# Performance work log

Measured on AMD Instinct MI355X. Metric: run time of the kernel, lower is better.

## Reference

```python
import jax, jax.numpy as jnp
import numpy as np

ALPHA = 1.0          # temperature of the Bayesian DP (init kwarg alpha)
NEG = -1e9           # -inf surrogate, safe in fp32/bf16


def conv1d_same(x, w, b):
    # x: [B, T, Cin], w: [K, Cin, Cout], 'SAME' padding, stride 1
    y = jax.lax.conv_general_dilated(x, w, window_strides=(1,), padding='SAME',
                                     dimension_numbers=('NWC', 'WIO', 'NWC'))
    return y + b


def postnet(x, ws, bs):
    # Tacotron-style conv PostNet: n_conv conv1d layers with tanh (dropout=0, eval mode)
    for w, b in zip(ws, bs):
        x = jnp.tanh(conv1d_same(x, w, b))
    return x


def bayesian_dp(W, alpha):
    """Monotonic-alignment Bayesian DP (Gumbel propagation).

    W: [B, T, S] node weights on the alignment grid (T = mel time, S = text).
    Each node (t, s) has two parents: (t-1, s) [stay] and (t-1, s-1) [advance].
      mu[t,s] = W[t,s] + (1/alpha) * logsumexp(alpha*mu[t-1,s], alpha*mu[t-1,s-1])
      pi[t,s] = softmax over the two parents -> [B, T, S, 2]
    """
    B, T, S = W.shape
    m0 = W[:, 0] + jnp.where(jnp.arange(S) == 0, 0.0, NEG)   # path must start at (0,0)
    pi0 = jnp.broadcast_to(jnp.array([1.0, 0.0], W.dtype), (B, S, 2))

    def step(prev, w_t):
        # prev: [B, S] = mu[t-1]; shifted: mu[t-1, s-1]
        shifted = jnp.concatenate([jnp.full((B, 1), NEG, prev.dtype), prev[:, :-1]], axis=1)
        stacked = jnp.stack([prev, shifted], axis=-1)         # [B, S, 2]
        m = w_t + jax.nn.logsumexp(alpha * stacked, axis=-1) / alpha
        pi_t = jax.nn.softmax(alpha * stacked, axis=-1)
        return m, (m, pi_t)

    _, (ms, pis) = jax.lax.scan(step, m0, jnp.swapaxes(W, 0, 1)[1:])  # scan over T-1
    mu = jnp.concatenate([m0[:, None], jnp.swapaxes(ms, 0, 1)], axis=1)    # [B, T, S]
    pi = jnp.concatenate([pi0[:, None], jnp.swapaxes(pis, 0, 1)], axis=1)  # [B, T, S, 2]
    return mu, pi


def setup_inputs() -> dict:
    key = jax.random.key(0)
    ks = jax.random.split(key, 6)
    B, T, S = 32, 2000, 400
    NMELS, H, K = 80, 256, 5
    inputs = jax.random.normal(ks[0], (B, T, NMELS), dtype=jnp.float32)
    src_enc = jax.random.normal(ks[1], (B, S, H), dtype=jnp.float32)
    mask = jnp.ones((B, T, S), dtype=jnp.float32)
    w1 = jax.random.normal(ks[2], (K, NMELS, H), dtype=jnp.float32) * 0.05
    w2 = jax.random.normal(ks[3], (K, H, H), dtype=jnp.float32) * 0.05
    w3 = jax.random.normal(ks[4], (K, H, H), dtype=jnp.float32) * 0.05
    b1 = jnp.zeros((H,), jnp.float32)
    b2 = jnp.zeros((H,), jnp.float32)
    b3 = jnp.zeros((H,), jnp.float32)
    return {"inputs": inputs, "src_enc": src_enc, "mask": mask,
            "w1": w1, "b1": b1, "w2": w2, "b2": b2, "w3": w3, "b3": b3}


def reference(inputs, src_enc, mask, w1, b1, w2, b2, w3, b3):
    # PostNet over mel frames -> spec embeddings matching src_enc dim
    Wspec = postnet(inputs, [w1, w2, w3], [b1, b2, b3])       # [B, T, H]
    # attention score grid
    W = jnp.einsum('bth,bsh->bts', Wspec, src_enc)            # [B, T, S]
    alignments = jax.nn.softmax(W, axis=1)                    # softmax over mel-time (dim 1)
    mu, pi = bayesian_dp(alignments * mask, ALPHA)
    return mu, pi, alignments, Wspec
```

## Files before the change

kernel.cpp:

```cpp
#include <hip/hip_runtime.h>
#include <hip/hip_bf16.h>

#define B_ 32
#define T_ 2000
#define S_ 400
#define C0_ 80
#define H_ 256

static constexpr float NEGV = -1e9f;
static constexpr int NMU  = B_ * T_ * S_;
static constexpr int NPI  = 2 * NMU;

typedef _Float16 f16x8 __attribute__((ext_vector_type(8)));
typedef float    f32x4 __attribute__((ext_vector_type(4)));

__global__ __launch_bounds__(256)
void wprep(const float* __restrict__ w, _Float16* __restrict__ wcat,
           int CIN, int CPAD)
{
  const int tot = 256 * 5 * CPAD;
  int idx = blockIdx.x * 256 + threadIdx.x;
  if (idx >= tot) return;
  int co  = idx / (5 * CPAD);
  int rem = idx - co * (5 * CPAD);
  int k   = rem / CPAD;
  int ci  = rem - k * CPAD;
  float v = (ci < CIN) ? w[((size_t)k * CIN + ci) * H_ + co] : 0.f;
  wcat[idx] = (_Float16)v;
}

__global__ __launch_bounds__(256)
void ecast(const float* __restrict__ e, _Float16* __restrict__ ef)
{
  const int n4 = B_ * S_ * H_ / 4;
  int idx = blockIdx.x * 256 + threadIdx.x;
  if (idx >= n4) return;
  float4 v = ((const float4*)e)[idx];
  _Float16* d = ef + (size_t)idx * 4;
  d[0] = (_Float16)v.x; d[1] = (_Float16)v.y;
  d[2] = (_Float16)v.z; d[3] = (_Float16)v.w;
}

template<int CIN, int CPAD, bool INF32, bool OUTF32>
__global__ __launch_bounds__(256)
void conv_mfma(const void* __restrict__ xin, const _Float16* __restrict__ wcat,
               const float* __restrict__ bias, void* __restrict__ yout)
{
  constexpr int KK  = 5 * CPAD;
  constexpr int NS  = KK / 32;
  constexpr int STR = CPAD + 8;
  __shared__ _Float16 xs[68 * STR];
  const int b   = blockIdx.y;
  const int t0  = blockIdx.x * 64;
  const int tid = threadIdx.x;
  const int w   = tid >> 6;
  const int l   = tid & 63;

  if constexpr (INF32) {
    const float* xb = (const float*)xin + (size_t)b * T_ * CIN;
    constexpr int NG = CPAD / 4;
    for (int idx = tid; idx < 68 * NG; idx += 256) {
      int j = idx / NG, g = idx - j * NG;
      int t = t0 - 2 + j;
      int c = g * 4;
      float4 v = make_float4(0.f, 0.f, 0.f, 0.f);
      if (t >= 0 && t < T_ && c < CIN) v = *(const float4*)&xb[(size_t)t * CIN + c];
      _Float16* d = &xs[j * STR + c];
      d[0] = (_Float16)v.x; d[1] = (_Float16)v.y;
      d[2] = (_Float16)v.z; d[3] = (_Float16)v.w;
    }
  } else {
    const _Float16* xb = (const _Float16*)xin + (size_t)b * T_ * CIN;
    constexpr int NG = CPAD / 8;
    for (int idx = tid; idx < 68 * NG; idx += 256) {
      int j = idx / NG, g = idx - j * NG;
      int t = t0 - 2 + j;
      f16x8 v = {(_Float16)0,(_Float16)0,(_Float16)0,(_Float16)0,
                 (_Float16)0,(_Float16)0,(_Float16)0,(_Float16)0};
      if (t >= 0 && t < T_) v = *(const f16x8*)&xb[(size_t)t * CIN + g * 8];
      *(f16x8*)&xs[j * STR + g * 8] = v;
    }
  }
  __syncthreads();

  const int lr = l & 15;
  const int lk = (l >> 4) * 8;

  f32x4 acc[4][4];
  const f32x4 zz = {0.f, 0.f, 0.f, 0.f};
#pragma unroll
  for (int i = 0; i < 4; i++)
#pragma unroll
    for (int j = 0; j < 4; j++) acc[i][j] = zz;

  const _Float16* wbase = wcat + (size_t)(w * 64 + lr) * KK + lk;

  for (int kk = 0; kk < NS; kk++) {
    const int p  = kk * 32;
    const int k  = p / CPAD;
    const int ci = p - k * CPAD;
    f16x8 a0 = *(const f16x8*)&xs[( 0 + lr + k) * STR + ci + lk];
    f16x8 a1 = *(const f16x8*)&xs[(16 + lr + k) * STR + ci + lk];
    f16x8 a2 = *(const f16x8*)&xs[(32 + lr + k) * STR + ci + lk];
    f16x8 a3 = *(const f16x8*)&xs[(48 + lr + k) * STR + ci + lk];
    f16x8 w0 = *(const f16x8*)&wbase[(size_t)( 0) * KK + p];
    f16x8 w1 = *(const f16x8*)&wbase[(size_t)(16) * KK + p];
    f16x8 w2 = *(const f16x8*)&wbase[(size_t)(32) * KK + p];
    f16x8 w3 = *(const f16x8*)&wbase[(size_t)(48) * KK + p];
    acc[0][0] = __builtin_amdgcn_mfma_f32_16x16x32_f16(a0, w0, acc[0][0], 0, 0, 0);
    acc[0][1] = __builtin_amdgcn_mfma_f32_16x16x32_f16(a0, w1, acc[0][1], 0, 0, 0);
    acc[0][2] = __builtin_amdgcn_mfma_f32_16x16x32_f16(a0, w2, acc[0][2], 0, 0, 0);
    acc[0][3] = __builtin_amdgcn_mfma_f32_16x16x32_f16(a0, w3, acc[0][3], 0, 0, 0);
    acc[1][0] = __builtin_amdgcn_mfma_f32_16x16x32_f16(a1, w0, acc[1][0], 0, 0, 0);
    acc[1][1] = __builtin_amdgcn_mfma_f32_16x16x32_f16(a1, w1, acc[1][1], 0, 0, 0);
    acc[1][2] = __builtin_amdgcn_mfma_f32_16x16x32_f16(a1, w2, acc[1][2], 0, 0, 0);
    acc[1][3] = __builtin_amdgcn_mfma_f32_16x16x32_f16(a1, w3, acc[1][3], 0, 0, 0);
    acc[2][0] = __builtin_amdgcn_mfma_f32_16x16x32_f16(a2, w0, acc[2][0], 0, 0, 0);
    acc[2][1] = __builtin_amdgcn_mfma_f32_16x16x32_f16(a2, w1, acc[2][1], 0, 0, 0);
    acc[2][2] = __builtin_amdgcn_mfma_f32_16x16x32_f16(a2, w2, acc[2][2], 0, 0, 0);
    acc[2][3] = __builtin_amdgcn_mfma_f32_16x16x32_f16(a2, w3, acc[2][3], 0, 0, 0);
    acc[3][0] = __builtin_amdgcn_mfma_f32_16x16x32_f16(a3, w0, acc[3][0], 0, 0, 0);
    acc[3][1] = __builtin_amdgcn_mfma_f32_16x16x32_f16(a3, w1, acc[3][1], 0, 0, 0);
    acc[3][2] = __builtin_amdgcn_mfma_f32_16x16x32_f16(a3, w2, acc[3][2], 0, 0, 0);
    acc[3][3] = __builtin_amdgcn_mfma_f32_16x16x32_f16(a3, w3, acc[3][3], 0, 0, 0);
  }

#pragma unroll
  for (int ct = 0; ct < 4; ct++) {
    const int co = w * 64 + ct * 16 + lr;
    const float bv = bias[co];
#pragma unroll
    for (int tt = 0; tt < 4; tt++) {
#pragma unroll
      for (int r = 0; r < 4; r++) {
        const int t = t0 + tt * 16 + (l >> 4) * 4 + r;
        if (t < T_) {
          float v = tanhf(acc[tt][ct][r] + bv);
          if constexpr (OUTF32)
            ((float*)yout)[((size_t)b * T_ + t) * H_ + co] = v;
          else
            ((_Float16*)yout)[((size_t)b * T_ + t) * H_ + co] = (_Float16)v;
        }
      }
    }
  }
}

__global__ __launch_bounds__(256)
void einsum_mfma(const float* __restrict__ A, const _Float16* __restrict__ E,
                 float* __restrict__ Wg)
{
  constexpr int STR = H_ + 8;
  __shared__ _Float16 xs[64 * STR];
  const int b   = blockIdx.z;
  const int t0  = blockIdx.x * 64;
  const int s0  = blockIdx.y * 256;
  const int tid = threadIdx.x;
  const int w   = tid >> 6;
  const int l   = tid & 63;

  const float* Ab = A + (size_t)b * T_ * H_;
  for (int idx = tid; idx < 64 * 64; idx += 256) {
    int row = idx >> 6, g = idx & 63;
    int t = t0 + row;
    float4 v = make_float4(0.f, 0.f, 0.f, 0.f);
    if (t < T_) v = *(const float4*)&Ab[(size_t)t * H_ + 4 * g];
    _Float16* d = &xs[row * STR + 4 * g];
    d[0] = (_Float16)v.x; d[1] = (_Float16)v.y;
    d[2] = (_Float16)v.z; d[3] = (_Float16)v.w;
  }
  __syncthreads();

  const int lr = l & 15;
  const int lk = (l >> 4) * 8;

  f32x4 acc[4][4];
  const f32x4 zz = {0.f, 0.f, 0.f, 0.f};
#pragma unroll
  for (int i = 0; i < 4; i++)
#pragma unroll
    for (int j = 0; j < 4; j++) acc[i][j] = zz;

  const _Float16* Eb = E + (size_t)b * S_ * H_;
  const int sr = s0 + w * 64 + lr;
  const _Float16* e0 = Eb + (size_t)((sr      < S_) ? sr      : (S_ - 1)) * H_ + lk;
  const _Float16* e1 = Eb + (size_t)((sr + 16 < S_) ? sr + 16 : (S_ - 1)) * H_ + lk;
  const _Float16* e2 = Eb + (size_t)((sr + 32 < S_) ? sr + 32 : (S_ - 1)) * H_ + lk;
  const _Float16* e3 = Eb + (size_t)((sr + 48 < S_) ? sr + 48 : (S_ - 1)) * H_ + lk;

#pragma unroll
  for (int kk = 0; kk < 8; kk++) {
    const int p = kk * 32;
    f16x8 a0 = *(const f16x8*)&xs[( 0 + lr) * STR + p + lk];
    f16x8 a1 = *(const f16x8*)&xs[(16 + lr) * STR + p + lk];
    f16x8 a2 = *(const f16x8*)&xs[(32 + lr) * STR + p + lk];
    f16x8 a3 = *(const f16x8*)&xs[(48 + lr) * STR + p + lk];
    f16x8 w0 = *(const f16x8*)&e0[p];
    f16x8 w1 = *(const f16x8*)&e1[p];
    f16x8 w2 = *(const f16x8*)&e2[p];
    f16x8 w3 = *(const f16x8*)&e3[p];
    acc[0][0] = __builtin_amdgcn_mfma_f32_16x16x32_f16(a0, w0, acc[0][0], 0, 0, 0);
    acc[0][1] = __builtin_amdgcn_mfma_f32_16x16x32_f16(a0, w1, acc[0][1], 0, 0, 0);
    acc[0][2] = __builtin_amdgcn_mfma_f32_16x16x32_f16(a0, w2, acc[0][2], 0, 0, 0);
    acc[0][3] = __builtin_amdgcn_mfma_f32_16x16x32_f16(a0, w3, acc[0][3], 0, 0, 0);
    acc[1][0] = __builtin_amdgcn_mfma_f32_16x16x32_f16(a1, w0, acc[1][0], 0, 0, 0);
    acc[1][1] = __builtin_amdgcn_mfma_f32_16x16x32_f16(a1, w1, acc[1][1], 0, 0, 0);
    acc[1][2] = __builtin_amdgcn_mfma_f32_16x16x32_f16(a1, w2, acc[1][2], 0, 0, 0);
    acc[1][3] = __builtin_amdgcn_mfma_f32_16x16x32_f16(a1, w3, acc[1][3], 0, 0, 0);
    acc[2][0] = __builtin_amdgcn_mfma_f32_16x16x32_f16(a2, w0, acc[2][0], 0, 0, 0);
    acc[2][1] = __builtin_amdgcn_mfma_f32_16x16x32_f16(a2, w1, acc[2][1], 0, 0, 0);
    acc[2][2] = __builtin_amdgcn_mfma_f32_16x16x32_f16(a2, w2, acc[2][2], 0, 0, 0);
    acc[2][3] = __builtin_amdgcn_mfma_f32_16x16x32_f16(a2, w3, acc[2][3], 0, 0, 0);
    acc[3][0] = __builtin_amdgcn_mfma_f32_16x16x32_f16(a3, w0, acc[3][0], 0, 0, 0);
    acc[3][1] = __builtin_amdgcn_mfma_f32_16x16x32_f16(a3, w1, acc[3][1], 0, 0, 0);
    acc[3][2] = __builtin_amdgcn_mfma_f32_16x16x32_f16(a3, w2, acc[3][2], 0, 0, 0);
    acc[3][3] = __builtin_amdgcn_mfma_f32_16x16x32_f16(a3, w3, acc[3][3], 0, 0, 0);
  }

  float* Wb = Wg + (size_t)b * T_ * S_;
#pragma unroll
  for (int ct = 0; ct < 4; ct++) {
    const int s = s0 + w * 64 + ct * 16 + lr;
    if (s < S_) {
#pragma unroll
      for (int tt = 0; tt < 4; tt++) {
#pragma unroll
        for (int r = 0; r < 4; r++) {
          const int t = t0 + tt * 16 + (l >> 4) * 4 + r;
          if (t < T_) Wb[(size_t)t * S_ + s] = acc[tt][ct][r];
        }
      }
    }
  }
}

__global__ __launch_bounds__(256)
void softmax_stats(const float* __restrict__ Wg, float* __restrict__ statsOut)
{
  const int b  = blockIdx.y;
  const int tx = threadIdx.x & 63;
  const int ty = threadIdx.x >> 6;
  const int s  = blockIdx.x * 64 + tx;
  const bool act = (s < S_);
  float m = -1e30f, l = 0.f;
  if (act) {
    const float* col = Wg + (size_t)b * T_ * S_ + s;
#pragma unroll 4
    for (int t = ty; t < T_; t += 4) {
      float v  = col[(size_t)t * S_];
      float nm = fmaxf(m, v);
      l = l * __expf(m - nm) + __expf(v - nm);
      m = nm;
    }
  }
  __shared__ float rm[4][64], rl[4][64];
  rm[ty][tx] = m; rl[ty][tx] = l;
  __syncthreads();
  if (ty == 0 && act) {
    float M = rm[0][tx];
#pragma unroll
    for (int q = 1; q < 4; q++) M = fmaxf(M, rm[q][tx]);
    float L = 0.f;
#pragma unroll
    for (int q = 0; q < 4; q++) L += rl[q][tx] * __expf(rm[q][tx] - M);
    statsOut[(size_t)b * S_ + s] = M + __logf(L);
  }
}

__global__ __launch_bounds__(256)
void norm_kernel(float* __restrict__ al, const float* __restrict__ Mk,
                 const float* __restrict__ stats, float* __restrict__ wdp)
{
  constexpr float C2 = 1.44269504f;
  const int gid = blockIdx.x * 256 + threadIdx.x;
  if (gid >= NMU / 4) return;
  const int b   = gid / (T_ * S_ / 4);
  const int rem = gid - b * (T_ * S_ / 4);
  const int s4  = rem % (S_ / 4);
  const float4 st4 = *(const float4*)&stats[(size_t)b * S_ + 4 * s4];
  float4 r = ((const float4*)al)[gid];
  float4 k = ((const float4*)Mk)[gid];
  float4 a;
  a.x = __expf(r.x - st4.x);
  a.y = __expf(r.y - st4.y);
  a.z = __expf(r.z - st4.z);
  a.w = __expf(r.w - st4.w);
  ((float4*)al)[gid] = a;
  ((float4*)wdp)[gid] = make_float4(a.x * k.x * C2, a.y * k.y * C2,
                                    a.z * k.z * C2, a.w * k.w * C2);
}

__global__ __launch_bounds__(256, 1)
void dp_skew2(const float* Wdp, float* muOut, float* piOut)
{
  __shared__ float ring[64 * S_];
  __shared__ float bnd[32][4];
  const int b = blockIdx.x;
  const int w = threadIdx.x >> 6;
  const int l = threadIdx.x & 63;
  const int lc = (l < 50) ? l : 49;
  const bool act = (l < 50);
  const int sc = 100 * w + 2 * lc;

  const float* wb  = Wdp   + (size_t)b * T_ * S_;
  float*       mub = muOut + (size_t)b * T_ * S_;
  float*       pib = piOut + (size_t)(2 * b) * T_ * S_;

  constexpr float LN2  = 0.693147181f;
  constexpr float NEGN = -1.44269504e9f;

#define DMA(row)                                                            \
  { const char* s_ = (const char*)(wb + (size_t)(row) * S_);                \
    char* d_ = (char*)ring + (((row) & 63) * 1600);                         \
    __builtin_amdgcn_global_load_lds(                                       \
      (const __attribute__((address_space(1))) void*)(s_ + l * 16),         \
      (__attribute__((address_space(3))) void*)(d_ + l * 16), 16, 0, 0);    \
    if (l < 36)                                                             \
      __builtin_amdgcn_global_load_lds(                                     \
        (const __attribute__((address_space(1))) void*)(s_ + 1024 + l*16),  \
        (__attribute__((address_space(3))) void*)(d_ + 1024 + l*16), 16, 0, 0); }

#pragma unroll
  for (int i = 0; i < 6; ++i) { const int r0 = 6 * w + i; DMA(r0) }
  asm volatile("s_waitcnt vmcnt(0)" ::: "memory");
  __syncthreads();

  float n0 = NEGN, n1 = NEGN;

  for (int p = 0; p <= 253; ++p) {
    __builtin_amdgcn_s_barrier();
    const int j = p - w - 1;

    {
      const int dr = 8 * p + 24 + 2 * w;
      if (dr < T_) DMA(dr)
      const int dr1 = dr + 1;
      if (dr1 < T_) DMA(dr1)
    }

    if (p == w) {
      float2 c0v = *(const float2*)&ring[sc];
      n0 = c0v.x + ((sc == 0) ? 0.f : NEGN);
      n1 = c0v.y + NEGN;
      if (act) {
        *(float2*)&mub[sc] = make_float2(n0 * LN2, n1 * LN2);
        *(float4*)&pib[2 * sc] = make_float4(1.f, 0.f, 1.f, 0.f);
      }
      if (l == 49) bnd[0][w] = n1;
    } else if (j >= 0 && j <= 249) {
      const int tb = 8 * j + 1;
      float2 cur[8];
      float  bq[8];
#pragma unroll
      for (int k = 0; k < 8; ++k) {
        const int t = tb + k;
        cur[k] = (t < T_) ? *(const float2*)&ring[(t & 63) * S_ + sc]
                          : make_float2(0.f, 0.f);
        bq[k] = (w > 0) ? bnd[(t - 1) & 31][w - 1] : NEGN;
      }
      float* mrow = mub + (size_t)tb * S_ + sc;
      float* prow = pib + (size_t)tb * (2 * S_) + 2 * sc;
#pragma unroll
      for (int k = 0; k < 8; ++k) {
        const int t = tb + k;
        if (t < T_) {
          float sh = __shfl_up(n1, 1);
          float sft0 = (l == 0) ? bq[k] : sh;
          float d0 = n0 - sft0;
          float e0; asm("v_exp_f32 %0, %1" : "=v"(e0) : "v"(-fabsf(d0)));
          float q0 = 1.f + e0;
          float lg0; asm("v_log_f32 %0, %1" : "=v"(lg0) : "v"(q0));
          float rc0; asm("v_rcp_f32 %0, %1" : "=v"(rc0) : "v"(q0));
          float p00 = (d0 >= 0.f) ? rc0 : 1.f - rc0;
          float nn0 = cur[k].x + fmaxf(n0, sft0) + lg0;
          float d1 = n1 - n0;
          float e1; asm("v_exp_f32 %0, %1" : "=v"(e1) : "v"(-fabsf(d1)));
          float q1 = 1.f + e1;
          float lg1; asm("v_log_f32 %0, %1" : "=v"(lg1) : "v"(q1));
          float rc1; asm("v_rcp_f32 %0, %1" : "=v"(rc1) : "v"(q1));
          float p01 = (d1 >= 0.f) ? rc1 : 1.f - rc1;
          float nn1 = cur[k].y + fmaxf(n1, n0) + lg1;
          if (act) {
            *(float2*)mrow = make_float2(nn0 * LN2, nn1 * LN2);
            *(float4*)prow = make_float4(p00, 1.f - p00, p01, 1.f - p01);
          }
          n0 = nn0; n1 = nn1;
          if (l == 49) bnd[t & 31][w] = n1;
        }
        mrow += S_;
        prow += 2 * S_;
      }
    }
    asm volatile("s_waitcnt lgkmcnt(0)" ::: "memory");
    asm volatile("s_waitcnt vmcnt(56)" ::: "memory");
  }
#undef DMA
}

extern "C" void kernel_launch(void* const* d_in, const int* in_sizes, int n_in,
                              void* d_out, int out_size, void* d_ws, size_t ws_size,
                              hipStream_t stream)
{
  (void)in_sizes; (void)n_in; (void)out_size; (void)d_ws; (void)ws_size;
  const float* x   = (const float*)d_in[0];
  const float* enc = (const float*)d_in[1];
  const float* msk = (const float*)d_in[2];
  const float* w1  = (const float*)d_in[3];
  const float* b1  = (const float*)d_in[4];
  const float* w2  = (const float*)d_in[5];
  const float* b2  = (const float*)d_in[6];
  const float* w3  = (const float*)d_in[7];
  const float* b3  = (const float*)d_in[8];

  float* out = (float*)d_out;
  float* mu  = out;
  float* pi  = out + NMU;
  float* al  = out + NMU + NPI;
  float* wsp = out + NMU + NPI + NMU;

  _Float16*  h1  = (_Float16*)(pi + 26000000);
  _Float16*  h2  = (_Float16*)(pi + 35000000);
  _Float16*  wc1 = (_Float16*)(pi + 44000000);
  _Float16*  wc2 = (_Float16*)(pi + 44100000);
  _Float16*  wc3 = (_Float16*)(pi + 44300000);
  _Float16*  encf = (_Float16*)(pi + 44600000);
  float*     pistats = pi + NPI - 13056;

  hipLaunchKernelGGL(wprep, dim3((256*5*96 +255)/256), dim3(256), 0, stream, w1, wc1, C0_, 96);
  hipLaunchKernelGGL(wprep, dim3((256*5*256+255)/256), dim3(256), 0, stream, w2, wc2, H_, 256);
  hipLaunchKernelGGL(wprep, dim3((256*5*256+255)/256), dim3(256), 0, stream, w3, wc3, H_, 256);
  hipLaunchKernelGGL(ecast, dim3(B_*S_*H_/4/256), dim3(256), 0, stream, enc, encf);

  dim3 cgrid((T_ + 63) / 64, B_);
  hipLaunchKernelGGL((conv_mfma<C0_,  96, true,  false>), cgrid, dim3(256), 0, stream,
                     (const void*)x,  wc1, b1, (void*)h1);
  hipLaunchKernelGGL((conv_mfma<H_,  256, false, false>), cgrid, dim3(256), 0, stream,
                     (const void*)h1, wc2, b2, (void*)h2);
  hipLaunchKernelGGL((conv_mfma<H_,  256, false, true >), cgrid, dim3(256), 0, stream,
                     (const void*)h2, wc3, b3, (void*)wsp);

  hipLaunchKernelGGL(einsum_mfma, dim3((T_ + 63) / 64, (S_ + 255) / 256, B_), dim3(256),
                     0, stream, wsp, encf, al);
  hipLaunchKernelGGL(softmax_stats, dim3((S_ + 63) / 64, B_), dim3(256), 0, stream, al, pistats);
  hipLaunchKernelGGL(norm_kernel, dim3(NMU / 4 / 256), dim3(256), 0, stream, al, msk, pistats, mu);
  hipLaunchKernelGGL(dp_skew2, dim3(B_), dim3(256), 0, stream, mu, mu, pi);
}
```

Measured before the change: 1.073 ms.

## Fuse softmax column statistics into einsum epilogue with partial max/sum reduction

The einsum kernel now computes per-tile column max and sum-of-exp from its accumulator registers. It combines them across lanes with xor shuffles and writes partial stats for each of the 32 time blocks. A small stats_reduce kernel then merges these partials into a log-sum-exp per (b, s). This removes the separate softmax_stats pass, which reread the whole 25.6M-element score grid with strided column access. It adds exp work and two scratch buffers to the einsum epilogue.

```diff
diff --git a/kernel.cpp b/kernel.cpp
--- a/kernel.cpp
+++ b/kernel.cpp
@@ -148,7 +148,8 @@
 
 __global__ __launch_bounds__(256)
 void einsum_mfma(const float* __restrict__ A, const _Float16* __restrict__ E,
-                 float* __restrict__ Wg)
+                 float* __restrict__ Wg,
+                 float* __restrict__ pm, float* __restrict__ pl)
 {
   constexpr int STR = H_ + 8;
   __shared__ _Float16 xs[64 * STR];
@@ -232,39 +233,61 @@
       }
     }
   }
-}
-
-__global__ __launch_bounds__(256)
-void softmax_stats(const float* __restrict__ Wg, float* __restrict__ statsOut)
-{
-  const int b  = blockIdx.y;
-  const int tx = threadIdx.x & 63;
-  const int ty = threadIdx.x >> 6;
-  const int s  = blockIdx.x * 64 + tx;
-  const bool act = (s < S_);
-  float m = -1e30f, l = 0.f;
-  if (act) {
-    const float* col = Wg + (size_t)b * T_ * S_ + s;
+
+  const int tblk = blockIdx.x;
+#pragma unroll
+  for (int ct = 0; ct < 4; ct++) {
+    float M = -3e38f;
+#pragma unroll
+    for (int tt = 0; tt < 4; tt++)
+#pragma unroll
+      for (int r = 0; r < 4; r++) {
+        const int t = t0 + tt * 16 + (l >> 4) * 4 + r;
+        if (t < T_) M = fmaxf(M, acc[tt][ct][r]);
+      }
+    float L = 0.f;
+#pragma unroll
+    for (int tt = 0; tt < 4; tt++)
+#pragma unroll
+      for (int r = 0; r < 4; r++) {
+        const int t = t0 + tt * 16 + (l >> 4) * 4 + r;
+        if (t < T_) L += __expf(acc[tt][ct][r] - M);
+      }
+#pragma unroll
+    for (int mk = 16; mk <= 32; mk <<= 1) {
+      float Mo = __shfl_xor(M, mk);
+      float Lo = __shfl_xor(L, mk);
+      float Mn = fmaxf(M, Mo);
+      L = L * __expf(M - Mn) + Lo * __expf(Mo - Mn);
+      M = Mn;
+    }
+    if ((l >> 4) == 0) {
+      const int s = s0 + w * 64 + ct * 16 + lr;
+      if (s < S_) {
+        pm[((size_t)b * 32 + tblk) * S_ + s] = M;
+        pl[((size_t)b * 32 + tblk) * S_ + s] = L;
+      }
+    }
+  }
+}
+
+__global__ __launch_bounds__(256)
+void stats_reduce(const float* __restrict__ pm, const float* __restrict__ pl,
+                  float* __restrict__ statsOut)
+{
+  int idx = blockIdx.x * 256 + threadIdx.x;
+  if (idx >= B_ * S_) return;
+  int b = idx / S_, s = idx - b * S_;
+  float M = -3e38f, L = 0.f;
 #pragma unroll 4
-    for (int t = ty; t < T_; t += 4) {
-      float v  = col[(size_t)t * S_];
-      float nm = fmaxf(m, v);
-      l = l * __expf(m - nm) + __expf(v - nm);
-      m = nm;
-    }
-  }
-  __shared__ float rm[4][64], rl[4][64];
-  rm[ty][tx] = m; rl[ty][tx] = l;
-  __syncthreads();
-  if (ty == 0 && act) {
-    float M = rm[0][tx];
-#pragma unroll
-    for (int q = 1; q < 4; q++) M = fmaxf(M, rm[q][tx]);
-    float L = 0.f;
-#pragma unroll
-    for (int q = 0; q < 4; q++) L += rl[q][tx] * __expf(rm[q][tx] - M);
-    statsOut[(size_t)b * S_ + s] = M + __logf(L);
-  }
+  for (int k = 0; k < 32; k++) {
+    float m = pm[((size_t)b * 32 + k) * S_ + s];
+    float l = pl[((size_t)b * 32 + k) * S_ + s];
+    float Mn = fmaxf(M, m);
+    L = L * __expf(M - Mn) + l * __expf(m - Mn);
+    M = Mn;
+  }
+  statsOut[(size_t)b * S_ + s] = M + __logf(L);
 }
 
 __global__ __launch_bounds__(256)
@@ -424,6 +447,8 @@
   _Float16*  wc2 = (_Float16*)(pi + 44100000);
   _Float16*  wc3 = (_Float16*)(pi + 44300000);
   _Float16*  encf = (_Float16*)(pi + 44600000);
+  float*     pm   = pi + 46300000;
+  float*     pl   = pi + 47200000;
   float*     pistats = pi + NPI - 13056;
 
   hipLaunchKernelGGL(wprep, dim3((256*5*96 +255)/256), dim3(256), 0, stream, w1, wc1, C0_, 96);
@@ -440,8 +465,9 @@
                      (const void*)h2, wc3, b3, (void*)wsp);
 
   hipLaunchKernelGGL(einsum_mfma, dim3((T_ + 63) / 64, (S_ + 255) / 256, B_), dim3(256),
-                     0, stream, wsp, encf, al);
-  hipLaunchKernelGGL(softmax_stats, dim3((S_ + 63) / 64, B_), dim3(256), 0, stream, al, pistats);
+                     0, stream, wsp, encf, al, pm, pl);
+  hipLaunchKernelGGL(stats_reduce, dim3((B_ * S_ + 255) / 256), dim3(256), 0, stream,
+                     pm, pl, pistats);
   hipLaunchKernelGGL(norm_kernel, dim3(NMU / 4 / 256), dim3(256), 0, stream, al, msk, pistats, mu);
   hipLaunchKernelGGL(dp_skew2, dim3(B_), dim3(256), 0, stream, mu, mu, pi);
 }
```

New measurement: 1.039 ms. 1.03x faster.
